# Kernel tuning notes

Measured on AMD Instinct MI355X. Metric: run time of the kernel, lower is better.

## Reference

```python
import jax, jax.numpy as jnp
import numpy as np

N_HEADS = 16
D_EMB = 1024
D_HEAD = D_EMB // N_HEADS


def setup_inputs() -> dict:
    key = jax.random.key(0)
    ks = jax.random.split(key, 5)
    scale = 1.0 / np.sqrt(D_EMB)
    x = jax.random.normal(ks[0], (4, 2048, D_EMB), dtype=jnp.float32)
    W_in = jax.random.normal(ks[1], (3 * D_EMB, D_EMB), dtype=jnp.float32) * scale
    b_in = jax.random.normal(ks[2], (3 * D_EMB,), dtype=jnp.float32) * 0.01
    W_out = jax.random.normal(ks[3], (D_EMB, D_EMB), dtype=jnp.float32) * scale
    b_out = jax.random.normal(ks[4], (D_EMB,), dtype=jnp.float32) * 0.01
    return {"x": x, "W_in": W_in, "b_in": b_in, "W_out": W_out, "b_out": b_out}


def reference(x, W_in, b_in, W_out, b_out):
    b, s, d = x.shape
    qkv = x @ W_in.T + b_in  # [b, s, 3d]
    q, k, v = jnp.split(qkv, 3, axis=-1)
    def heads(t):
        return t.reshape(b, s, N_HEADS, D_HEAD).transpose(0, 2, 1, 3)  # [b,h,s,dh]
    q, k, v = heads(q), heads(k), heads(v)
    scores = jnp.einsum('bhqd,bhkd->bhqk', q, k)
    causal = jnp.tril(jnp.ones((s, s), dtype=bool))  # keep lower-triangular incl diag
    scores = jnp.where(causal, scores, -jnp.inf)
    scores = scores / np.sqrt(D_HEAD).astype(np.float32)
    w = jax.nn.softmax(scores, axis=-1)
    out = jnp.einsum('bhqk,bhkd->bhqd', w, v)  # [b,h,s,dh]
    out = out.transpose(0, 2, 1, 3).reshape(b, s, d)
    return out @ W_out.T + b_out
```

## Files before the change

### kernel.cpp

```cpp
#include <hip/hip_runtime.h>
#include <hip/hip_bf16.h>
#include <cstdint>


typedef float  floatx4  __attribute__((ext_vector_type(4)));
typedef __bf16 bf16x8   __attribute__((ext_vector_type(8)));
typedef __bf16 bf16x4   __attribute__((ext_vector_type(4)));
typedef short  shortx4  __attribute__((ext_vector_type(4)));
typedef unsigned int   uint32x2 __attribute__((ext_vector_type(2)));
typedef unsigned short ushortx8 __attribute__((ext_vector_type(8)));

#define MFMA16(a,b,c) __builtin_amdgcn_mfma_f32_16x16x32_bf16(a, b, c, 0, 0, 0)

__device__ __forceinline__ floatx4 mfma_k16(bf16x4 a, bf16x4 b, floatx4 c) {
#if defined(__HIP_DEVICE_COMPILE__)
#if __has_builtin(__builtin_amdgcn_mfma_f32_16x16x16_bf16)
  return __builtin_amdgcn_mfma_f32_16x16x16_bf16(a, b, c, 0, 0, 0);
#elif __has_builtin(__builtin_amdgcn_mfma_f32_16x16x16bf16_1k)
  return __builtin_amdgcn_mfma_f32_16x16x16bf16_1k(
      __builtin_bit_cast(shortx4, a), __builtin_bit_cast(shortx4, b), c, 0, 0, 0);
#else
  floatx4 d;
  asm("v_mfma_f32_16x16x16_bf16 %0, %1, %2, %3"
      : "=v"(d)
      : "v"(__builtin_bit_cast(uint32x2, a)),
        "v"(__builtin_bit_cast(uint32x2, b)), "v"(c));
  return d;
#endif
#else
  (void)a; (void)b;
  return c;
#endif
}

#define C_SCALE 0.18033688011112042f
#define M_STATIC 16.0f

__device__ __forceinline__ void gload_lds16(const void* g, void* l) {
  __builtin_amdgcn_global_load_lds(
      (__attribute__((address_space(1))) void*)(g),
      (__attribute__((address_space(3))) void*)(l), 16, 0, 0);
}

#define N_X4    2097152
#define N_WIN4  786432
#define N_WOUT4 262144
#define N_B4    768
__global__ __launch_bounds__(256) void cast_fused(
    const float* __restrict__ x, const float* __restrict__ W_in,
    const float* __restrict__ W_out, const float* __restrict__ b_in,
    __bf16* __restrict__ xb, __bf16* __restrict__ Winb,
    __bf16* __restrict__ Woutb, float* __restrict__ bins) {
  int i = blockIdx.x * 256 + threadIdx.x;
  if (i < N_X4) {
    const float4 v = ((const float4*)x)[i];
    bf16x4 o;
    o.x = (__bf16)v.x; o.y = (__bf16)v.y; o.z = (__bf16)v.z; o.w = (__bf16)v.w;
    ((bf16x4*)xb)[i] = o;
  } else if (i < N_X4 + N_WIN4) {
    const int j = i - N_X4;
    const float s = (j < 262144) ? C_SCALE : 1.0f;
    const float4 v = ((const float4*)W_in)[j];
    bf16x4 o;
    o.x = (__bf16)(v.x * s); o.y = (__bf16)(v.y * s);
    o.z = (__bf16)(v.z * s); o.w = (__bf16)(v.w * s);
    ((bf16x4*)Winb)[j] = o;
  } else if (i < N_X4 + N_WIN4 + N_WOUT4) {
    const int j = i - N_X4 - N_WIN4;
    const float4 v = ((const float4*)W_out)[j];
    bf16x4 o;
    o.x = (__bf16)v.x; o.y = (__bf16)v.y; o.z = (__bf16)v.z; o.w = (__bf16)v.w;
    ((bf16x4*)Woutb)[j] = o;
  } else {
    const int j = i - N_X4 - N_WIN4 - N_WOUT4;
    const float s = (j < 256) ? C_SCALE : 1.0f;
    float4 v = ((const float4*)b_in)[j];
    v.x *= s; v.y *= s; v.z *= s; v.w *= s;
    ((float4*)bins)[j] = v;
  }
}

template <int MODE>
__global__ __launch_bounds__(256) void gemm_bt(
    const __bf16* __restrict__ A, const __bf16* __restrict__ B,
    const float* __restrict__ bias, void* __restrict__ Cout,
    __bf16* __restrict__ Vt, int M, int N, int K) {
  __shared__ __bf16 As[128 * 32];
  __shared__ __bf16 Bs[128 * 32];
  const int tid = threadIdx.x;
  const int wave = tid >> 6, lane = tid & 63;
  const int quad = lane >> 4, l15 = lane & 15;
  const int wm = (wave & 1) * 64, wn = (wave >> 1) * 64;
  const long row0 = (long)blockIdx.y * 128;
  const long col0 = (long)blockIdx.x * 128;

  floatx4 acc[4][4] = {};

  const int sr = wave * 16 + (lane >> 2);
  const int sc = (lane & 3) * 8;
  const __bf16* ga = A + (row0 + sr) * (long)K + sc;
  const __bf16* gb = B + (col0 + sr) * (long)K + sc;
  __bf16* lA = As + wave * 512 + lane * 8;
  __bf16* lB = Bs + wave * 512 + lane * 8;

  for (int k0 = 0; k0 < K; k0 += 32) {
    gload_lds16(ga,                lA);
    gload_lds16(ga + 64 * (long)K, lA + 2048);
    gload_lds16(gb,                lB);
    gload_lds16(gb + 64 * (long)K, lB + 2048);
    ga += 32; gb += 32;
    __syncthreads();

    bf16x8 af[4], bfr[4];
#pragma unroll
    for (int i = 0; i < 4; ++i)
      af[i] = *(const bf16x8*)(As + (wm + i * 16 + l15) * 32 + quad * 8);
#pragma unroll
    for (int j = 0; j < 4; ++j)
      bfr[j] = *(const bf16x8*)(Bs + (wn + j * 16 + l15) * 32 + quad * 8);
#pragma unroll
    for (int i = 0; i < 4; ++i)
#pragma unroll
      for (int j = 0; j < 4; ++j)
        acc[i][j] = MFMA16(af[i], bfr[j], acc[i][j]);
    __syncthreads();
  }

#pragma unroll
  for (int i = 0; i < 4; ++i) {
    const long r0 = row0 + wm + i * 16 + quad * 4;
#pragma unroll
    for (int j = 0; j < 4; ++j) {
      const long c = col0 + wn + j * 16 + l15;
      const float bv = bias[c];
      if (MODE == 0) {
#pragma unroll
        for (int reg = 0; reg < 4; ++reg)
          ((float*)Cout)[(r0 + reg) * (long)N + c] = acc[i][j][reg] + bv;
      } else {
        if (c < 2048) {
#pragma unroll
          for (int reg = 0; reg < 4; ++reg)
            ((__bf16*)Cout)[(r0 + reg) * (long)N + c] =
                (__bf16)(acc[i][j][reg] + bv);
        } else {
          const int cc = (int)c - 2048;
          const int hh = cc >> 6, dh = cc & 63;
          const int bb = (int)(r0 >> 11), s = (int)(r0 & 2047);
          bf16x4 pk;
#pragma unroll
          for (int reg = 0; reg < 4; ++reg)
            pk[reg] = (__bf16)(acc[i][j][reg] + bv);
          *(bf16x4*)(Vt + ((long)(bb * 16 + hh) * 64 + dh) * 2048 + s) = pk;
        }
      }
    }
  }
}

__global__ __launch_bounds__(256, 4) void flash_attn(
    const __bf16* __restrict__ qkv,
    const __bf16* __restrict__ Vt,
    __bf16* __restrict__ Out) {
  constexpr int S = 2048;
  const int h = blockIdx.y, b = blockIdx.z;
  const int x = (int)(blockIdx.x + 5 * blockIdx.z + 3 * blockIdx.y) & 15;
  const int qtA = x, qtB = 31 - x;
  const int kmaxA = qtA + 1;
  const int kmax  = qtB + 1;

  __shared__ __bf16 Ks[2][64 * 72];
  __shared__ __bf16 Vs[2][64 * 72];

  const int tid = threadIdx.x, wave = tid >> 6, lane = tid & 63;
  const int quad = lane >> 4, l15 = lane & 15;

  bf16x8 qf[2][2];
  {
    const long qrA = (long)(b * S + qtA * 64 + wave * 16 + l15) * 3072 + h * 64;
    const long qrB = (long)(b * S + qtB * 64 + wave * 16 + l15) * 3072 + h * 64;
    qf[0][0] = *(const bf16x8*)(qkv + qrA + quad * 8);
    qf[0][1] = *(const bf16x8*)(qkv + qrA + 32 + quad * 8);
    qf[1][0] = *(const bf16x8*)(qkv + qrB + quad * 8);
    qf[1][1] = *(const bf16x8*)(qkv + qrB + 32 + quad * 8);
  }

  bf16x4 ones4;
#pragma unroll
  for (int j = 0; j < 4; ++j) ones4[j] = (__bf16)1.0f;

  floatx4 oA[4] = {}, oB[4] = {};
  floatx4 lA = {0.f, 0.f, 0.f, 0.f}, lB = {0.f, 0.f, 0.f, 0.f};

  const int srow = tid >> 3;
  const int sc8 = (tid & 7) * 8;
  const __bf16* ka = qkv + ((long)(b * S) + srow) * 3072 + 1024 + h * 64 + sc8;
  const __bf16* va = Vt + ((long)(b * 16 + h) * 64 + srow) * S + sc8;
  const int sl = srow * 72 + sc8;

  ushortx8 kr0 = *(const ushortx8*)ka;
  ushortx8 kr1 = *(const ushortx8*)(ka + 32 * 3072);
  ushortx8 vr0 = *(const ushortx8*)va;
  ushortx8 vr1 = *(const ushortx8*)(va + 32 * (long)S);
  *(ushortx8*)(&Ks[0][sl]) = kr0;
  *(ushortx8*)(&Ks[0][sl + 32 * 72]) = kr1;
  *(ushortx8*)(&Vs[0][sl]) = vr0;
  *(ushortx8*)(&Vs[0][sl + 32 * 72]) = vr1;
  kr0 = *(const ushortx8*)(ka + 64 * 3072);
  kr1 = *(const ushortx8*)(ka + 96 * 3072);
  vr0 = *(const ushortx8*)(va + 64);
  vr1 = *(const ushortx8*)(va + 32 * (long)S + 64);
  __syncthreads();

  for (int kt = 0; kt < kmax; ++kt) {
    const int cur = kt & 1;
    if (kt + 1 < kmax) {
      *(ushortx8*)(&Ks[cur ^ 1][sl]) = kr0;
      *(ushortx8*)(&Ks[cur ^ 1][sl + 32 * 72]) = kr1;
      *(ushortx8*)(&Vs[cur ^ 1][sl]) = vr0;
      *(ushortx8*)(&Vs[cur ^ 1][sl + 32 * 72]) = vr1;
    }
    if (kt + 2 < kmax) {
      const long ko = (long)(kt + 2) * 64 * 3072;
      kr0 = *(const ushortx8*)(ka + ko);
      kr1 = *(const ushortx8*)(ka + ko + 32 * 3072);
      vr0 = *(const ushortx8*)(va + (kt + 2) * 64);
      vr1 = *(const ushortx8*)(va + 32 * (long)S + (kt + 2) * 64);
    }

    const bool actA = (kt < kmaxA);
    const bool partA = (kt == qtA);
    const bool partB = (kt == qtB);

    floatx4 svA[4], svB[4];
#pragma unroll
    for (int nb = 0; nb < 4; ++nb) {
      const bf16x8 k0 = *(const bf16x8*)(&Ks[cur][(nb * 16 + l15) * 72 + quad * 8]);
      const bf16x8 k1 = *(const bf16x8*)(&Ks[cur][(nb * 16 + l15) * 72 + 32 + quad * 8]);
      if (actA) {
        floatx4 z = {0.f, 0.f, 0.f, 0.f};
        z = MFMA16(k0, qf[0][0], z);
        z = MFMA16(k1, qf[0][1], z);
        svA[nb] = z;
      }
      {
        floatx4 z = {0.f, 0.f, 0.f, 0.f};
        z = MFMA16(k0, qf[1][0], z);
        z = MFMA16(k1, qf[1][1], z);
        svB[nb] = z;
      }
    }

    if (partA) {
      const int qg = qtA * 64 + wave * 16 + l15;
#pragma unroll
      for (int nb = 0; nb < 4; ++nb) {
        const int key0 = kt * 64 + nb * 16 + quad * 4;
#pragma unroll
        for (int r = 0; r < 4; ++r)
          if (key0 + r > qg) svA[nb][r] = -1.0e30f;
      }
    }
    if (partB) {
      const int qg = qtB * 64 + wave * 16 + l15;
#pragma unroll
      for (int nb = 0; nb < 4; ++nb) {
        const int key0 = kt * 64 + nb * 16 + quad * 4;
#pragma unroll
        for (int r = 0; r < 4; ++r)
          if (key0 + r > qg) svB[nb][r] = -1.0e30f;
      }
    }

    bf16x4 pfA[4], pfB[4];
    if (actA) {
#pragma unroll
      for (int nb = 0; nb < 4; ++nb)
#pragma unroll
        for (int r = 0; r < 4; ++r)
          pfA[nb][r] = (__bf16)exp2f(svA[nb][r] - M_STATIC);
#pragma unroll
      for (int c = 0; c < 4; ++c) lA = mfma_k16(ones4, pfA[c], lA);
    }
    {
#pragma unroll
      for (int nb = 0; nb < 4; ++nb)
#pragma unroll
        for (int r = 0; r < 4; ++r)
          pfB[nb][r] = (__bf16)exp2f(svB[nb][r] - M_STATIC);
#pragma unroll
      for (int c = 0; c < 4; ++c) lB = mfma_k16(ones4, pfB[c], lB);
    }

#pragma unroll
    for (int mb = 0; mb < 4; ++mb) {
#pragma unroll
      for (int c = 0; c < 4; ++c) {
        const bf16x4 vf = *(const bf16x4*)(&Vs[cur][(mb * 16 + l15) * 72 + c * 16 + quad * 4]);
        if (actA) oA[mb] = mfma_k16(vf, pfA[c], oA[mb]);
        oB[mb] = mfma_k16(vf, pfB[c], oB[mb]);
      }
    }
    __syncthreads();
  }

  {
    const float inv = 1.f / lA[0];
    const long row = (long)(b * S + qtA * 64 + wave * 16 + l15);
#pragma unroll
    for (int mb = 0; mb < 4; ++mb) {
      bf16x4 pk;
#pragma unroll
      for (int r = 0; r < 4; ++r) pk[r] = (__bf16)(oA[mb][r] * inv);
      *(bf16x4*)(Out + row * 1024 + h * 64 + mb * 16 + quad * 4) = pk;
    }
  }
  {
    const float inv = 1.f / lB[0];
    const long row = (long)(b * S + qtB * 64 + wave * 16 + l15);
#pragma unroll
    for (int mb = 0; mb < 4; ++mb) {
      bf16x4 pk;
#pragma unroll
      for (int r = 0; r < 4; ++r) pk[r] = (__bf16)(oB[mb][r] * inv);
      *(bf16x4*)(Out + row * 1024 + h * 64 + mb * 16 + quad * 4) = pk;
    }
  }
}

extern "C" void kernel_launch(void* const* d_in, const int* in_sizes, int n_in,
                              void* d_out, int out_size, void* d_ws, size_t ws_size,
                              hipStream_t stream) {
  const float* x     = (const float*)d_in[0];
  const float* W_in  = (const float*)d_in[1];
  const float* b_in  = (const float*)d_in[2];
  const float* W_out = (const float*)d_in[3];
  const float* b_out = (const float*)d_in[4];

  const int BS = 4 * 2048;
  const int D = 1024, N3 = 3072;

  char* w = (char*)d_ws;
  __bf16* xb    = (__bf16*)w;  w += (size_t)BS * D * 2;
  __bf16* Winb  = (__bf16*)w;  w += (size_t)N3 * D * 2;
  __bf16* Woutb = (__bf16*)w;  w += (size_t)D * D * 2;
  __bf16* qkvb  = (__bf16*)w;  w += (size_t)BS * N3 * 2;
  __bf16* Vtb   = (__bf16*)w;  w += (size_t)64 * 64 * 2048 * 2;
  __bf16* attnb = (__bf16*)w;  w += (size_t)BS * D * 2;
  float*  bins  = (float*)w;   w += (size_t)N3 * 4;

  const int castN = N_X4 + N_WIN4 + N_WOUT4 + N_B4;
  cast_fused<<<dim3(castN / 256), 256, 0, stream>>>(
      x, W_in, W_out, b_in, xb, Winb, Woutb, bins);

  gemm_bt<2><<<dim3(N3 / 128, BS / 128), 256, 0, stream>>>(
      xb, Winb, bins, (void*)qkvb, Vtb, BS, N3, D);

  flash_attn<<<dim3(16, 16, 4), 256, 0, stream>>>(qkvb, Vtb, attnb);

  gemm_bt<0><<<dim3(D / 128, BS / 128), 256, 0, stream>>>(
      attnb, Woutb, b_out, d_out, nullptr, BS, D, D);
}
```

Baseline: 288.4 us.

## Load K/V tiles directly to LDS with XOR-swizzled unpadded layout

Replaces the register-staged global-to-LDS copy of K and V tiles with direct global-to-LDS loads (gload_lds16), prefetching one tile ahead into the double buffer. The LDS tiles drop row padding and use an XOR swizzle on 16-byte groups to avoid bank conflicts on the MFMA operand reads. This frees the VGPRs that held the prefetch data, and the occupancy hint in launch bounds is removed. The risk is that the prefetch distance shrinks from two tiles to one, and the direct loads depend on the helper's wait semantics relative to the barrier.

```diff
diff --git a/kernel.cpp b/kernel.cpp
--- a/kernel.cpp
+++ b/kernel.cpp
@@ -158,7 +158,7 @@
   }
 }
 
-__global__ __launch_bounds__(256, 4) void flash_attn(
+__global__ __launch_bounds__(256) void flash_attn(
     const __bf16* __restrict__ qkv,
     const __bf16* __restrict__ Vt,
     __bf16* __restrict__ Out) {
@@ -169,11 +169,12 @@
   const int kmaxA = qtA + 1;
   const int kmax  = qtB + 1;
 
-  __shared__ __bf16 Ks[2][64 * 72];
-  __shared__ __bf16 Vs[2][64 * 72];
+  __shared__ __bf16 Ks[2][64 * 64];
+  __shared__ __bf16 Vs[2][64 * 64];
 
   const int tid = threadIdx.x, wave = tid >> 6, lane = tid & 63;
   const int quad = lane >> 4, l15 = lane & 15;
+  const int sx = l15 & 7;
 
   bf16x8 qf[2][2];
   {
@@ -192,40 +193,29 @@
   floatx4 oA[4] = {}, oB[4] = {};
   floatx4 lA = {0.f, 0.f, 0.f, 0.f}, lB = {0.f, 0.f, 0.f, 0.f};
 
-  const int srow = tid >> 3;
-  const int sc8 = (tid & 7) * 8;
-  const __bf16* ka = qkv + ((long)(b * S) + srow) * 3072 + 1024 + h * 64 + sc8;
-  const __bf16* va = Vt + ((long)(b * 16 + h) * 64 + srow) * S + sc8;
-  const int sl = srow * 72 + sc8;
-
-  ushortx8 kr0 = *(const ushortx8*)ka;
-  ushortx8 kr1 = *(const ushortx8*)(ka + 32 * 3072);
-  ushortx8 vr0 = *(const ushortx8*)va;
-  ushortx8 vr1 = *(const ushortx8*)(va + 32 * (long)S);
-  *(ushortx8*)(&Ks[0][sl]) = kr0;
-  *(ushortx8*)(&Ks[0][sl + 32 * 72]) = kr1;
-  *(ushortx8*)(&Vs[0][sl]) = vr0;
-  *(ushortx8*)(&Vs[0][sl + 32 * 72]) = vr1;
-  kr0 = *(const ushortx8*)(ka + 64 * 3072);
-  kr1 = *(const ushortx8*)(ka + 96 * 3072);
-  vr0 = *(const ushortx8*)(va + 64);
-  vr1 = *(const ushortx8*)(va + 32 * (long)S + 64);
+  const int rl = wave * 8 + (lane >> 3);
+  const int lg = (lane & 7) ^ (rl & 7);
+  const __bf16* kg0 = qkv + ((long)(b * S) + rl) * 3072 + 1024 + h * 64 + lg * 8;
+  const __bf16* kg1 = kg0 + 32 * 3072;
+  const __bf16* vg0 = Vt + ((long)(b * 16 + h) * 64 + rl) * 2048 + lg * 8;
+  const __bf16* vg1 = vg0 + 32 * 2048;
+  const int slel = wave * 512 + lane * 8;
+
+  gload_lds16(kg0, &Ks[0][slel]);
+  gload_lds16(kg1, &Ks[0][slel + 2048]);
+  gload_lds16(vg0, &Vs[0][slel]);
+  gload_lds16(vg1, &Vs[0][slel + 2048]);
   __syncthreads();
 
   for (int kt = 0; kt < kmax; ++kt) {
     const int cur = kt & 1;
     if (kt + 1 < kmax) {
-      *(ushortx8*)(&Ks[cur ^ 1][sl]) = kr0;
-      *(ushortx8*)(&Ks[cur ^ 1][sl + 32 * 72]) = kr1;
-      *(ushortx8*)(&Vs[cur ^ 1][sl]) = vr0;
-      *(ushortx8*)(&Vs[cur ^ 1][sl + 32 * 72]) = vr1;
-    }
-    if (kt + 2 < kmax) {
-      const long ko = (long)(kt + 2) * 64 * 3072;
-      kr0 = *(const ushortx8*)(ka + ko);
-      kr1 = *(const ushortx8*)(ka + ko + 32 * 3072);
-      vr0 = *(const ushortx8*)(va + (kt + 2) * 64);
-      vr1 = *(const ushortx8*)(va + 32 * (long)S + (kt + 2) * 64);
+      const long ko = (long)(kt + 1) * 64 * 3072;
+      const int vo = (kt + 1) * 64;
+      gload_lds16(kg0 + ko, &Ks[cur ^ 1][slel]);
+      gload_lds16(kg1 + ko, &Ks[cur ^ 1][slel + 2048]);
+      gload_lds16(vg0 + vo, &Vs[cur ^ 1][slel]);
+      gload_lds16(vg1 + vo, &Vs[cur ^ 1][slel + 2048]);
     }
 
     const bool actA = (kt < kmaxA);
@@ -235,8 +225,9 @@
     floatx4 svA[4], svB[4];
 #pragma unroll
     for (int nb = 0; nb < 4; ++nb) {
-      const bf16x8 k0 = *(const bf16x8*)(&Ks[cur][(nb * 16 + l15) * 72 + quad * 8]);
-      const bf16x8 k1 = *(const bf16x8*)(&Ks[cur][(nb * 16 + l15) * 72 + 32 + quad * 8]);
+      const int krow = (nb * 16 + l15) * 64;
+      const bf16x8 k0 = *(const bf16x8*)(&Ks[cur][krow + (quad ^ sx) * 8]);
+      const bf16x8 k1 = *(const bf16x8*)(&Ks[cur][krow + ((4 + quad) ^ sx) * 8]);
       if (actA) {
         floatx4 z = {0.f, 0.f, 0.f, 0.f};
         z = MFMA16(k0, qf[0][0], z);
@@ -294,9 +285,12 @@
 
 #pragma unroll
     for (int mb = 0; mb < 4; ++mb) {
+      const int vrow = (mb * 16 + l15) * 64;
 #pragma unroll
       for (int c = 0; c < 4; ++c) {
-        const bf16x4 vf = *(const bf16x4*)(&Vs[cur][(mb * 16 + l15) * 72 + c * 16 + quad * 4]);
+        const int pg = (2 * c + (quad >> 1)) ^ sx;
+        const bf16x4 vf =
+            *(const bf16x4*)(&Vs[cur][vrow + pg * 8 + (quad & 1) * 4]);
         if (actA) oA[mb] = mfma_k16(vf, pfA[c], oA[mb]);
         oB[mb] = mfma_k16(vf, pfB[c], oB[mb]);
       }
```

Result: slower. 492.7 us (+70.8%).
